# Performance work log

Measured on AMD Instinct MI355X. Metric: run time of the kernel, lower is better.

The kernel has to match this reference:

```python
import jax, jax.numpy as jnp
import numpy as np

B, XDIM, TWIN, INCH = 1024, 62, 10, 128
MID, OUT, K, K1, LIN, HC = 256, 512, 3, 10, 512, 4
EPS = 1e-5

REGIONS = [
    list(range(0, 5)),
    list(range(5, 8)) + list(range(14, 17)),
    list(range(8, 11)) + list(range(17, 20)),
    list(range(11, 14)) + list(range(20, 23)),
    list(range(23, 26)) + list(range(32, 35)),
    list(range(26, 29)) + list(range(35, 38)),
    list(range(29, 32)) + list(range(38, 41)),
    list(range(41, 44)) + list(range(50, 52)) + list(range(57, 58)),
    list(range(44, 47)) + list(range(52, 55)) + list(range(58, 61)),
    list(range(47, 50)) + list(range(55, 57)) + list(range(61, 62)),
]


def setup_inputs() -> dict:
    key = jax.random.key(0)
    ks = jax.random.split(key, 40)
    n = lambda k, s, sc=0.02: jax.random.normal(k, s, jnp.float32) * sc
    inp = {
        "x": jax.random.normal(ks[0], (B, XDIM, TWIN, INCH), jnp.float32),
        "tfe_w": n(ks[1], (XDIM, TWIN)),          # depthwise Conv2d (10,1) weight, squeezed
        "tfe_b": jnp.zeros((XDIM,), jnp.float32),
        "cheby1_w": n(ks[2], (K, INCH, OUT)),
        "A": n(ks[3], (XDIM, XDIM)),
        "cheby2_w": n(ks[4], (K, MID, OUT)),
        "A1": n(ks[5], (K1, K1)),
        "b_gate": jnp.float32(1.0),
        "c_gate": jnp.float32(1.0),
        "region_b": jnp.zeros((K1, MID), jnp.float32),
        "hc_w1": n(ks[6], (OUT * 72, LIN)),
        "hc_b1": jnp.zeros((LIN,), jnp.float32),
        "bn1_g": jnp.ones((LIN,), jnp.float32),
        "bn1_b": jnp.zeros((LIN,), jnp.float32),
        "hc_w2": n(ks[7], (LIN, LIN // 2)),
        "hc_b2": jnp.zeros((LIN // 2,), jnp.float32),
        "bn2_g": jnp.ones((LIN // 2,), jnp.float32),
        "bn2_b": jnp.zeros((LIN // 2,), jnp.float32),
        "hc_w3": n(ks[8], (LIN // 2, HC)),
        "hc_b3": jnp.zeros((HC,), jnp.float32),
    }
    for i, idx in enumerate(REGIONS):
        inp[f"rw{i+1}"] = n(ks[10 + i], (MID, INCH, len(idx)))
    return inp


def _cheby(x, L, Ws):
    # sum_k  S_k @ x @ W_k  with S_0 = I, S_k = S_{k-1} @ L ; then ReLU
    S = jnp.eye(L.shape[0], dtype=x.dtype)
    res = jnp.zeros(x.shape[:2] + (Ws.shape[-1],), x.dtype)
    for k in range(Ws.shape[0]):
        res = res + jnp.einsum("nm,bmt,to->bno", S, x, Ws[k])
        S = S @ L
    return jax.nn.relu(res)


def _bn(h, g, b):
    mu = h.mean(axis=0)
    v = h.var(axis=0)  # biased, training-mode BatchNorm1d
    return (h - mu) * jax.lax.rsqrt(v + EPS) * g + b


def _forward(x, tfe_w, tfe_b, cheby1_w, A, cheby2_w, A1, b_gate, c_gate,
             rw1, rw2, rw3, rw4, rw5, rw6, rw7, rw8, rw9, rw10, region_b,
             hc_w1, hc_b1, bn1_g, bn1_b, hc_w2, hc_b2, bn2_g, bn2_b, hc_w3, hc_b3):
    # variance gate (torch.var default: unbiased)
    sigma = jnp.var(x, axis=2, ddof=1)                              # (B, 62, INCH)
    g_tfe = jnp.einsum("bcit,ci->bct", x, tfe_w) + tfe_b[None, :, None]
    g = g_tfe * jnp.exp(-sigma)                                      # (B, 62, INCH)

    g1 = _cheby(g, A, cheby1_w)                                      # (B, 62, OUT)

    rws = [rw1, rw2, rw3, rw4, rw5, rw6, rw7, rw8, rw9, rw10]
    RG = []
    for i, (idx, w) in enumerate(zip(REGIONS, rws)):
        reg = g[:, jnp.asarray(idx), :]                              # (B, L, INCH)
        RG.append(jnp.einsum("blc,mcl->bm", reg, w) + region_b[i])   # Conv1d, full-width kernel
    g2in = jnp.stack(RG, axis=1)                                     # (B, 10, MID)
    g2 = _cheby(g2in, A1, cheby2_w)                                  # (B, 10, OUT)

    att = jnp.concatenate([b_gate * g1, c_gate * g2], axis=1)        # (B, 72, OUT)
    cat = jnp.concatenate([g1, g2], axis=1)
    out = jax.nn.softmax(att, axis=1) * cat
    out = out.reshape(out.shape[0], -1)                              # (B, 72*OUT)

    h = jax.nn.gelu(_bn(out @ hc_w1 + hc_b1, bn1_g, bn1_b), approximate=False)
    h = jax.nn.gelu(_bn(h @ hc_w2 + hc_b2, bn2_g, bn2_b), approximate=False)
    h = h @ hc_w3 + hc_b3
    return jax.nn.softmax(h, axis=1)


def reference(x, tfe_w, tfe_b, cheby1_w, A, cheby2_w, A1, b_gate, c_gate,
              rw1, rw2, rw3, rw4, rw5, rw6, rw7, rw8, rw9, rw10, region_b,
              hc_w1, hc_b1, bn1_g, bn1_b, hc_w2, hc_b2, bn2_g, bn2_b, hc_w3, hc_b3):
    return _forward(x, tfe_w, tfe_b, cheby1_w, A, cheby2_w, A1, b_gate, c_gate,
                    rw1, rw2, rw3, rw4, rw5, rw6, rw7, rw8, rw9, rw10, region_b,
                    hc_w1, hc_b1, bn1_g, bn1_b, hc_w2, hc_b2, bn2_g, bn2_b, hc_w3, hc_b3)
```

## Files before the change

### kernel.cpp

```cpp
#include <hip/hip_runtime.h>
#include <math.h>


__constant__ int cOrder[62] = {
  0,1,2,3,4,
  5,6,7,14,15,16,
  8,9,10,17,18,19,
  11,12,13,20,21,22,
  23,24,25,32,33,34,
  26,27,28,35,36,37,
  29,30,31,38,39,40,
  41,42,43,50,51,57,
  44,45,46,52,53,54,58,59,60,
  47,48,49,55,56,61
};
__constant__ int cPos[62] = {
  0,1,2,3,4, 5,6,7, 11,12,13, 17,18,19, 8,9,10, 14,15,16, 20,21,22,
  23,24,25, 29,30,31, 35,36,37, 26,27,28, 32,33,34, 38,39,40,
  41,42,43, 47,48,49, 56,57,58, 44,45, 50,51,52, 59,60, 46, 53,54,55, 61
};
__constant__ int cRegK[10]   = {640,768,768,768,768,768,768,768,1152,768};
__constant__ int cRegCum[10] = {0,640,1408,2176,2944,3712,4480,5248,6016,7168};

struct Ptr10 { const float* p[10]; };

typedef __attribute__((ext_vector_type(8))) short bf16x8;
typedef __attribute__((ext_vector_type(4))) float f32x4;

__device__ __forceinline__ float gelu_exact(float v){
  return 0.5f * v * (1.0f + erff(v * 0.70710678118654752f));
}
__device__ __forceinline__ unsigned short f2bf(float f){
  unsigned u = __float_as_uint(f);
  unsigned r = (u + 0x7fffu + ((u >> 16) & 1u)) >> 16;
  return (unsigned short)r;
}
__device__ __forceinline__ float bf2f(unsigned short u){
  return __uint_as_float(((unsigned)u) << 16);
}
__device__ __forceinline__ void load_lds16(const unsigned short* g, unsigned short* l){
  __builtin_amdgcn_global_load_lds(
      (const __attribute__((address_space(1))) void*)g,
      (__attribute__((address_space(3))) void*)l, 16, 0, 0);
}

template<bool RELU>
__global__ __launch_bounds__(256) void k_mfma(
    const unsigned short* __restrict__ A, long lda,
    const unsigned short* __restrict__ BT, long ldb,
    void* __restrict__ Cv, int ldc, int kPerZ, long cStrideZ, int mcCount){
  __shared__ unsigned short As[128*32];
  __shared__ unsigned short Bs[128*32];
  int mt, nt, zt;
  if (mcCount){
    int id = blockIdx.x;
    int c = ((id >> 6) << 3) + (id & 7);
    int member = (id >> 3) & 7;
    zt = c / mcCount;
    int mc = c - zt*mcCount;
    mt = mc*2 + (member >> 2);
    nt = member & 3;
  } else { mt = blockIdx.x; nt = blockIdx.y; zt = blockIdx.z; }
  int tid = threadIdx.x;
  int wave = tid >> 6, lane = tid & 63;
  int m0 = mt * 128, n0 = nt * 128;
  int kStart = zt * kPerZ;
  int waveM = wave >> 1, waveN = wave & 1;
  int lr = lane >> 2, ch = lane & 3;
  int quad = lane >> 4, mrow = lane & 15;
  int swe = ((quad ^ (mrow & 3)) << 3);

  int rA0 = wave*32 + lr;
  int rA1 = rA0 + 16;
  int ce  = ((ch ^ (rA0 & 3)) << 3);
  const unsigned short* gA0 = A  + (long)(m0 + rA0)*lda + kStart + ce;
  const unsigned short* gA1 = A  + (long)(m0 + rA1)*lda + kStart + ce;
  const unsigned short* gB0 = BT + (long)(n0 + rA0)*ldb + kStart + ce;
  const unsigned short* gB1 = BT + (long)(n0 + rA1)*ldb + kStart + ce;
  unsigned short* lA0 = &As[(wave*32)*32];
  unsigned short* lA1 = &As[(wave*32+16)*32];
  unsigned short* lB0 = &Bs[(wave*32)*32];
  unsigned short* lB1 = &Bs[(wave*32+16)*32];

  f32x4 acc[4][4] = {};
  int nIter = kPerZ >> 5;
  for (int it = 0; it < nIter; ++it){
    long ko = (long)it << 5;
    load_lds16(gA0 + ko, lA0);
    load_lds16(gA1 + ko, lA1);
    load_lds16(gB0 + ko, lB0);
    load_lds16(gB1 + ko, lB1);
    __syncthreads();
    bf16x8 af[4], bfr[4];
#pragma unroll
    for (int mi = 0; mi < 4; mi++)
      af[mi] = *(const bf16x8*)&As[(waveM*64 + mi*16 + mrow)*32 + swe];
#pragma unroll
    for (int ni = 0; ni < 4; ni++)
      bfr[ni] = *(const bf16x8*)&Bs[(waveN*64 + ni*16 + mrow)*32 + swe];
#pragma unroll
    for (int mi = 0; mi < 4; mi++)
#pragma unroll
      for (int ni = 0; ni < 4; ni++)
        acc[mi][ni] = __builtin_amdgcn_mfma_f32_16x16x32_bf16(
            af[mi], bfr[ni], acc[mi][ni], 0, 0, 0);
    __syncthreads();
  }
  if (RELU){
    unsigned short* C = (unsigned short*)Cv;
#pragma unroll
    for (int mi = 0; mi < 4; mi++)
#pragma unroll
      for (int ni = 0; ni < 4; ni++){
        int col = n0 + waveN*64 + ni*16 + mrow;
#pragma unroll
        for (int r = 0; r < 4; r++){
          int row = m0 + waveM*64 + mi*16 + quad*4 + r;
          C[(long)row*ldc + col] = f2bf(fmaxf(acc[mi][ni][r], 0.f));
        }
      }
  } else {
    float* C = (float*)Cv + (long)zt * cStrideZ;
#pragma unroll
    for (int mi = 0; mi < 4; mi++)
#pragma unroll
      for (int ni = 0; ni < 4; ni++){
        int col = n0 + waveN*64 + ni*16 + mrow;
#pragma unroll
        for (int r = 0; r < 4; r++){
          int row = m0 + waveM*64 + mi*16 + quad*4 + r;
          C[(long)row*ldc + col] = acc[mi][ni][r];
        }
      }
  }
}
template __global__ void k_mfma<true>(const unsigned short*, long, const unsigned short*, long, void*, int, int, long, int);
template __global__ void k_mfma<false>(const unsigned short*, long, const unsigned short*, long, void*, int, int, long, int);

__global__ __launch_bounds__(256) void k_mfma_region(
    const unsigned short* __restrict__ ARb,
    const unsigned short* __restrict__ RWT,
    const float* __restrict__ regb, float* __restrict__ g2in){
  __shared__ unsigned short As[128*32];
  __shared__ unsigned short Bs[128*32];
  int z = blockIdx.z;
  int K = cRegK[z];
  int cumk = cRegCum[z];
  const unsigned short* A  = ARb + cumk;
  const unsigned short* BT = RWT + (long)cumk*256;
  long lda = 7936, ldb = K;
  int tid = threadIdx.x;
  int wave = tid >> 6, lane = tid & 63;
  int m0 = blockIdx.x * 128, n0 = blockIdx.y * 128;
  int waveM = wave >> 1, waveN = wave & 1;
  int lr = lane >> 2, ch = lane & 3;
  int quad = lane >> 4, mrow = lane & 15;
  int swe = ((quad ^ (mrow & 3)) << 3);

  int rA0 = wave*32 + lr;
  int rA1 = rA0 + 16;
  int ce  = ((ch ^ (rA0 & 3)) << 3);
  const unsigned short* gA0 = A  + (long)(m0 + rA0)*lda + ce;
  const unsigned short* gA1 = A  + (long)(m0 + rA1)*lda + ce;
  const unsigned short* gB0 = BT + (long)(n0 + rA0)*ldb + ce;
  const unsigned short* gB1 = BT + (long)(n0 + rA1)*ldb + ce;
  unsigned short* lA0 = &As[(wave*32)*32];
  unsigned short* lA1 = &As[(wave*32+16)*32];
  unsigned short* lB0 = &Bs[(wave*32)*32];
  unsigned short* lB1 = &Bs[(wave*32+16)*32];

  f32x4 acc[4][4] = {};
  int nIter = K >> 5;
  for (int it = 0; it < nIter; ++it){
    long ko = (long)it << 5;
    load_lds16(gA0 + ko, lA0);
    load_lds16(gA1 + ko, lA1);
    load_lds16(gB0 + ko, lB0);
    load_lds16(gB1 + ko, lB1);
    __syncthreads();
    bf16x8 af[4], bfr[4];
#pragma unroll
    for (int mi = 0; mi < 4; mi++)
      af[mi] = *(const bf16x8*)&As[(waveM*64 + mi*16 + mrow)*32 + swe];
#pragma unroll
    for (int ni = 0; ni < 4; ni++)
      bfr[ni] = *(const bf16x8*)&Bs[(waveN*64 + ni*16 + mrow)*32 + swe];
#pragma unroll
    for (int mi = 0; mi < 4; mi++)
#pragma unroll
      for (int ni = 0; ni < 4; ni++)
        acc[mi][ni] = __builtin_amdgcn_mfma_f32_16x16x32_bf16(
            af[mi], bfr[ni], acc[mi][ni], 0, 0, 0);
    __syncthreads();
  }
#pragma unroll
  for (int mi = 0; mi < 4; mi++)
#pragma unroll
    for (int ni = 0; ni < 4; ni++){
      int col = n0 + waveN*64 + ni*16 + mrow;
      float bias = regb[z*256 + col];
#pragma unroll
      for (int r = 0; r < 4; r++){
        int row = m0 + waveM*64 + mi*16 + quad*4 + r;
        g2in[(long)row*2560 + z*256 + col] = acc[mi][ni][r] + bias;
      }
    }
}

__global__ __launch_bounds__(256) void k_front(
    const float* __restrict__ s0, unsigned short* __restrict__ d0,
    const float* __restrict__ s1, unsigned short* __restrict__ d1,
    const float* __restrict__ s2, unsigned short* __restrict__ d2,
    const float* __restrict__ s3, unsigned short* __restrict__ d3,
    Ptr10 rws, unsigned short* __restrict__ RWT,
    const float* __restrict__ Amat, float* __restrict__ AT,
    float* __restrict__ A2T,
    const float* __restrict__ x, const float* __restrict__ tw,
    const float* __restrict__ tb, unsigned short* __restrict__ arb,
    unsigned short* __restrict__ xcat, float* __restrict__ sumz){
  __shared__ float smem[64*65];
  int id = blockIdx.x;
  int tid = threadIdx.x;
  if (id >= 15342){
    *(float4*)(sumz + tid*4) = make_float4(0.f,0.f,0.f,0.f);
    return;
  }
  if (id >= 7406){
    int q = id - 7406;
    int r = tid >> 5, j = tid & 31;
    int idx = q*8 + r;
    int b = idx / 62, n = idx - b*62;
    const float4* xp = (const float4*)(x + (long)idx*1280) + j;
    float sx=0.f,sy=0.f,sz=0.f,sw=0.f;
    float qx=0.f,qy=0.f,qz=0.f,qw=0.f;
    float gx=0.f,gy=0.f,gz=0.f,gw=0.f;
#pragma unroll
    for (int i = 0; i < 10; i++){
      float4 v = xp[i*32];
      float w = tw[n*10+i];
      sx+=v.x; sy+=v.y; sz+=v.z; sw+=v.w;
      qx=fmaf(v.x,v.x,qx); qy=fmaf(v.y,v.y,qy);
      qz=fmaf(v.z,v.z,qz); qw=fmaf(v.w,v.w,qw);
      gx=fmaf(v.x,w,gx); gy=fmaf(v.y,w,gy);
      gz=fmaf(v.z,w,gz); gw=fmaf(v.w,w,gw);
    }
    float tbn = tb[n];
    float mx_=sx*0.1f, my_=sy*0.1f, mz_=sz*0.1f, mw_=sw*0.1f;
    float rx = (gx+tbn)*expf(-(qx-10.f*mx_*mx_)*(1.f/9.f));
    float ry = (gy+tbn)*expf(-(qy-10.f*my_*my_)*(1.f/9.f));
    float rz = (gz+tbn)*expf(-(qz-10.f*mz_*mz_)*(1.f/9.f));
    float rw = (gw+tbn)*expf(-(qw-10.f*mw_*mw_)*(1.f/9.f));
    ushort4 u = make_ushort4(f2bf(rx), f2bf(ry), f2bf(rz), f2bf(rw));
    *(ushort4*)(arb  + (long)b*7936  + cPos[n]*128 + j*4) = u;
    *(ushort4*)(xcat + (long)b*23808 + n*384       + j*4) = u;
    return;
  }
  if (id < 7344 && id >= 4784){
    int q = id - 4784;
    int z = q >> 8, m = q & 255;
    int K = cRegK[z], L = K >> 7;
    const float* rw = rws.p[z] + (long)m*K;
    unsigned short* dst = RWT + (long)cRegCum[z]*256 + (long)m*K;
    for (int i = tid; i < K; i += 256) smem[i] = rw[i];
    __syncthreads();
    for (int k = tid; k < K; k += 256){
      int l = k >> 7, c = k & 127;
      dst[k] = f2bf(smem[c*L + l]);
    }
    return;
  }
  if (id >= 7344){
    int r = id - 7344, c = tid;
    if (c < 62) smem[c] = Amat[r*62 + c];
    __syncthreads();
    if (c < 62){
      AT[c*62 + r] = smem[c];
      float s = 0.f;
      for (int t = 0; t < 62; t++) s = fmaf(smem[t], Amat[t*62 + c], s);
      A2T[c*62 + r] = s;
    }
    return;
  }
  const float* src; unsigned short* dst; int R, C, rt, ct;
  if (id < 4608){ src=s0; dst=d0; R=36864; C=512; rt=id>>3;  ct=id&7; }
  else if (id < 4640){ int q=id-4608; src=s1; dst=d1; R=512; C=256; rt=q>>2; ct=q&3; }
  else if (id < 4688){ int q=id-4640; src=s2; dst=d2; R=384; C=512; rt=q>>3; ct=q&7; }
  else { int q=id-4688; src=s3; dst=d3; R=768; C=512; rt=q>>3; ct=q&7; }
  int r0 = rt*64, c0 = ct*64;
  int rr = tid >> 2, cb = (tid & 3) << 2;
#pragma unroll
  for (int i = 0; i < 4; i++){
    int cc = cb + i*16;
    float4 v = *(const float4*)(src + (long)(r0+rr)*C + c0 + cc);
    smem[rr*65+cc+0]=v.x; smem[rr*65+cc+1]=v.y;
    smem[rr*65+cc+2]=v.z; smem[rr*65+cc+3]=v.w;
  }
  __syncthreads();
  int cc = tid >> 2, rb = (tid & 3) << 2;
#pragma unroll
  for (int i = 0; i < 4; i++){
    int r = rb + i*16;
    ushort4 u = make_ushort4(f2bf(smem[(r+0)*65+cc]), f2bf(smem[(r+1)*65+cc]),
                             f2bf(smem[(r+2)*65+cc]), f2bf(smem[(r+3)*65+cc]));
    *(ushort4*)(dst + (long)(c0+cc)*R + r0 + r) = u;
  }
}

__global__ __launch_bounds__(256) void k_spread2(
    const unsigned short* __restrict__ ARb, const float* __restrict__ AT,
    const float* __restrict__ A2T, unsigned short* __restrict__ xcat){
  __shared__ float sgn[7936];
  int b = blockIdx.x, tid = threadIdx.x;
  for (int i = tid; i < 7936; i += 256){
    int p = i >> 7, c = i & 127;
    sgn[cOrder[p]*128 + c] = bf2f(ARb[(long)b*7936 + i]);
  }
  __syncthreads();
  int c = tid & 127, mat = tid >> 7;
  const float* MT = mat ? A2T : AT;
  float acc[62];
#pragma unroll
  for (int n = 0; n < 62; n++) acc[n] = 0.f;
  for (int m = 0; m < 62; m++){
    float gv = sgn[m*128 + c];
    const float* Mp = MT + m*62;
#pragma unroll
    for (int n = 0; n < 62; n++) acc[n] = fmaf(Mp[n], gv, acc[n]);
  }
  long base = (long)b*23808 + (mat+1)*128 + c;
#pragma unroll
  for (int n = 0; n < 62; n++) xcat[base + (long)n*384] = f2bf(acc[n]);
}

__global__ __launch_bounds__(256) void k_x2cat(
    const float* __restrict__ g2in, const float* __restrict__ A1,
    unsigned short* __restrict__ X2){
  __shared__ float sg[2560];
  __shared__ float sA1[100];
  __shared__ float sA2[100];
  int b = blockIdx.x, tid = threadIdx.x;
  for (int i = tid; i < 2560; i += 256) sg[i] = g2in[(long)b*2560 + i];
  if (tid < 100) sA1[tid] = A1[tid];
  __syncthreads();
  if (tid < 100){
    int n = tid/10, m = tid - n*10;
    float a = 0.f;
#pragma unroll
    for (int t = 0; t < 10; t++) a = fmaf(sA1[n*10+t], sA1[t*10+m], a);
    sA2[tid] = a;
  }
  __syncthreads();
  for (int i = tid; i < 2560; i += 256){
    int n = i >> 8, t = i & 255;
    float v1 = 0.f, v2 = 0.f;
#pragma unroll
    for (int m = 0; m < 10; m++){
      float gv = sg[(m<<8) + t];
      v1 = fmaf(sA1[n*10+m], gv, v1);
      v2 = fmaf(sA2[n*10+m], gv, v2);
    }
    long base = (long)b*7680 + n*768;
    X2[base + t]       = f2bf(sg[i]);
    X2[base + 256 + t] = f2bf(v1);
    X2[base + 512 + t] = f2bf(v2);
  }
}

__global__ __launch_bounds__(256) void k_softcat(
    const unsigned short* __restrict__ g1, const unsigned short* __restrict__ g2,
    const float* __restrict__ bg_, const float* __restrict__ cg_,
    unsigned short* __restrict__ outb){
  int b = blockIdx.x;
  int o = blockIdx.y*256 + threadIdx.x;
  float v[72];
  const unsigned short* p1 = g1 + (long)b*62*512 + o;
#pragma unroll
  for (int j = 0; j < 62; j++) v[j] = bf2f(p1[j*512]);
  const unsigned short* p2 = g2 + (long)b*10*512 + o;
#pragma unroll
  for (int j = 0; j < 10; j++) v[62+j] = bf2f(p2[j*512]);
  float bg = *bg_, cg = *cg_;
  float mx = -1e30f;
#pragma unroll
  for (int j = 0; j < 72; j++){
    float av = (j < 62 ? bg : cg) * v[j];
    mx = fmaxf(mx, av);
  }
  float sum = 0.f;
#pragma unroll
  for (int j = 0; j < 72; j++){
    float e = expf((j < 62 ? bg : cg) * v[j] - mx);
    sum += e;
    v[j] = e * v[j];
  }
  float inv = 1.f / sum;
  unsigned short* op = outb + (long)b*36864 + o;
#pragma unroll
  for (int j = 0; j < 72; j++) op[j*512] = f2bf(v[j] * inv);
}

__global__ __launch_bounds__(256) void k_reduce_stats(
    const float4* __restrict__ P, float4* __restrict__ h1,
    float* __restrict__ sum, float* __restrict__ ssq){
  __shared__ float4 ls[128], ls2[128];
  int c  = threadIdx.x & 127;
  int rr = threadIdx.x >> 7;
  int r0 = blockIdx.x * 8;
  float4 s1 = make_float4(0.f,0.f,0.f,0.f);
  float4 s2 = make_float4(0.f,0.f,0.f,0.f);
#pragma unroll
  for (int k = 0; k < 4; k++){
    int row = r0 + rr + 2*k;
    long idx = (long)row*128 + c;
    float4 v = make_float4(0.f,0.f,0.f,0.f);
#pragma unroll
    for (int s = 0; s < 16; s++){
      float4 p = P[(long)s*131072 + idx];
      v.x += p.x; v.y += p.y; v.z += p.z; v.w += p.w;
    }
    h1[idx] = v;
    s1.x += v.x; s1.y += v.y; s1.z += v.z; s1.w += v.w;
    s2.x = fmaf(v.x,v.x,s2.x); s2.y = fmaf(v.y,v.y,s2.y);
    s2.z = fmaf(v.z,v.z,s2.z); s2.w = fmaf(v.w,v.w,s2.w);
  }
  if (rr){ ls[c] = s1; ls2[c] = s2; }
  __syncthreads();
  if (!rr){
    float4 o1 = ls[c], o2 = ls2[c];
    atomicAdd(&sum[c*4+0], s1.x+o1.x); atomicAdd(&sum[c*4+1], s1.y+o1.y);
    atomicAdd(&sum[c*4+2], s1.z+o1.z); atomicAdd(&sum[c*4+3], s1.w+o1.w);
    atomicAdd(&ssq[c*4+0], s2.x+o2.x); atomicAdd(&ssq[c*4+1], s2.y+o2.y);
    atomicAdd(&ssq[c*4+2], s2.z+o2.z); atomicAdd(&ssq[c*4+3], s2.w+o2.w);
  }
}

__global__ __launch_bounds__(256) void k_bngelu(
    const float* __restrict__ h1, const float* __restrict__ sum,
    const float* __restrict__ ssq, const float* __restrict__ gam,
    const float* __restrict__ bet, unsigned short* __restrict__ h1b){
  int base = (blockIdx.x*256 + threadIdx.x) * 4;
  int j = base & 511;
  float4 v = *(const float4*)(h1 + base);
  float mu0 = sum[j+0]*(1.f/1024.f), mu1 = sum[j+1]*(1.f/1024.f);
  float mu2 = sum[j+2]*(1.f/1024.f), mu3 = sum[j+3]*(1.f/1024.f);
  float rs0 = rsqrtf(ssq[j+0]*(1.f/1024.f) - mu0*mu0 + 1e-5f);
  float rs1 = rsqrtf(ssq[j+1]*(1.f/1024.f) - mu1*mu1 + 1e-5f);
  float rs2 = rsqrtf(ssq[j+2]*(1.f/1024.f) - mu2*mu2 + 1e-5f);
  float rs3 = rsqrtf(ssq[j+3]*(1.f/1024.f) - mu3*mu3 + 1e-5f);
  ushort4 u;
  u.x = f2bf(gelu_exact((v.x - mu0)*rs0*gam[j+0] + bet[j+0]));
  u.y = f2bf(gelu_exact((v.y - mu1)*rs1*gam[j+1] + bet[j+1]));
  u.z = f2bf(gelu_exact((v.z - mu2)*rs2*gam[j+2] + bet[j+2]));
  u.w = f2bf(gelu_exact((v.w - mu3)*rs3*gam[j+3] + bet[j+3]));
  *(ushort4*)(h1b + base) = u;
}

__global__ __launch_bounds__(256) void k_stats2r(
    const float* __restrict__ P2, float* __restrict__ h2,
    float* __restrict__ mu, float* __restrict__ rs){
  __shared__ float lsm[256], lss[256];
  int j0 = blockIdx.x * 8;
  int jj = threadIdx.x & 7, bg = threadIdx.x >> 3;
  float s = 0.f, s2 = 0.f;
#pragma unroll 4
  for (int it = 0; it < 32; it++){
    int row = it*32 + bg;
    float v = 0.f;
#pragma unroll
    for (int sp = 0; sp < 4; sp++)
      v += P2[((long)sp*1024 + row)*256 + j0 + jj];
    h2[(long)row*256 + j0 + jj] = v;
    s += v; s2 = fmaf(v, v, s2);
  }
  lsm[threadIdx.x] = s; lss[threadIdx.x] = s2;
  __syncthreads();
  if (threadIdx.x < 8){
    float a = lsm[threadIdx.x], a2 = lss[threadIdx.x];
    for (int g = 1; g < 32; g++){ a += lsm[g*8 + threadIdx.x]; a2 += lss[g*8 + threadIdx.x]; }
    float m = a * (1.f/1024.f);
    float var = a2 * (1.f/1024.f) - m*m;
    mu[j0 + threadIdx.x] = m;
    rs[j0 + threadIdx.x] = rsqrtf(var + 1e-5f);
  }
}

__global__ __launch_bounds__(256) void k_final(
    const float* __restrict__ h2, const float* __restrict__ mu,
    const float* __restrict__ rs, const float* __restrict__ gam,
    const float* __restrict__ bet, const float* __restrict__ w3,
    const float* __restrict__ b3, float* __restrict__ outp){
  int b = blockIdx.x, tid = threadIdx.x;
  float v = h2[(long)b*256 + tid];
  v = (v - mu[tid]) * rs[tid] * gam[tid] + bet[tid];
  v = gelu_exact(v);
  float4 w = ((const float4*)w3)[tid];
  float p0 = v*w.x, p1 = v*w.y, p2 = v*w.z, p3 = v*w.w;
#pragma unroll
  for (int o = 32; o > 0; o >>= 1){
    p0 += __shfl_down(p0, o);
    p1 += __shfl_down(p1, o);
    p2 += __shfl_down(p2, o);
    p3 += __shfl_down(p3, o);
  }
  __shared__ float red[4][4];
  int wv = tid >> 6;
  if ((tid & 63) == 0){ red[wv][0]=p0; red[wv][1]=p1; red[wv][2]=p2; red[wv][3]=p3; }
  __syncthreads();
  if (tid == 0){
    float l[4];
#pragma unroll
    for (int c = 0; c < 4; c++)
      l[c] = red[0][c]+red[1][c]+red[2][c]+red[3][c] + b3[c];
    float m = fmaxf(fmaxf(l[0], l[1]), fmaxf(l[2], l[3]));
    float e[4]; float sum = 0.f;
#pragma unroll
    for (int c = 0; c < 4; c++){ e[c] = expf(l[c]-m); sum += e[c]; }
    float inv = 1.f / sum;
#pragma unroll
    for (int c = 0; c < 4; c++) outp[(long)b*4 + c] = e[c]*inv;
  }
}

extern "C" void kernel_launch(void* const* d_in, const int* in_sizes, int n_in,
                              void* d_out, int out_size, void* d_ws, size_t ws_size,
                              hipStream_t stream){
  (void)n_in; (void)out_size; (void)ws_size;
  bool dictOrder = (in_sizes[9] == 2560);
  const float* x     = (const float*)d_in[0];
  const float* tfe_w = (const float*)d_in[1];
  const float* tfe_b = (const float*)d_in[2];
  const float* ch1w  = (const float*)d_in[3];
  const float* Amat  = (const float*)d_in[4];
  const float* ch2w  = (const float*)d_in[5];
  const float* A1mat = (const float*)d_in[6];
  const float* bgate = (const float*)d_in[7];
  const float* cgate = (const float*)d_in[8];
  const float* regb  = (const float*)d_in[dictOrder ? 9 : 19];
  int o = dictOrder ? 0 : 10;
  const float* hc_w1 = (const float*)d_in[10+o];
  const float* bn1g  = (const float*)d_in[12+o];
  const float* bn1b  = (const float*)d_in[13+o];
  const float* hc_w2 = (const float*)d_in[14+o];
  const float* bn2g  = (const float*)d_in[16+o];
  const float* bn2b  = (const float*)d_in[17+o];
  const float* hc_w3 = (const float*)d_in[18+o];
  const float* hc_b3 = (const float*)d_in[19+o];
  Ptr10 rws;
  for (int i = 0; i < 10; i++) rws.p[i] = (const float*)d_in[(dictOrder ? 20 : 9) + i];

  char* Wb = (char*)d_ws;
  unsigned short* ARb   = (unsigned short*)(Wb + 0);
  unsigned short* XCAT  = (unsigned short*)(Wb + 16252928);
  unsigned short* RWT   = (unsigned short*)(Wb + 65011712);
  float*          G2IN  = (float*)(Wb + 69074944);
  unsigned short* X2CAT = (unsigned short*)(Wb + 79560704);
  unsigned short* W1T   = (unsigned short*)(Wb + 95289344);
  unsigned short* WC1T  = (unsigned short*)(Wb + 133038080);
  unsigned short* WC2T  = (unsigned short*)(Wb + 133431296);
  unsigned short* G1    = (unsigned short*)(Wb + 134217728);
  unsigned short* G2    = (unsigned short*)(Wb + 199229440);
  unsigned short* OUTB  = (unsigned short*)(Wb + 0);
  float*          P     = (float*)(Wb + 209715200);
  float*          H1    = (float*)(Wb + 243269632);
  float*          H2    = (float*)(Wb + 245366784);
  float*          SUM1  = (float*)(Wb + 246415360);
  float*          SSQ1  = SUM1 + 512;
  float*          MU2   = SUM1 + 1024;
  float*          RS2   = SUM1 + 1280;
  float*          AT    = (float*)(Wb + 246423552);
  float*          A2T   = (float*)(Wb + 246439040);
  unsigned short* W2T   = (unsigned short*)(Wb + 246454528);
  unsigned short* H1B   = (unsigned short*)(Wb + 246716928);

  k_front<<<15343, 256, 0, stream>>>(hc_w1, W1T, hc_w2, W2T, ch1w, WC1T,
                                     ch2w, WC2T, rws, RWT, Amat, AT, A2T,
                                     x, tfe_w, tfe_b, ARb, XCAT, SUM1);
  k_spread2<<<1024, 256, 0, stream>>>(ARb, AT, A2T, XCAT);
  k_mfma_region<<<dim3(8,2,10), 256, 0, stream>>>(ARb, RWT, regb, G2IN);
  k_x2cat<<<1024, 256, 0, stream>>>(G2IN, A1mat, X2CAT);
  k_mfma<true><<<320, 256, 0, stream>>>(X2CAT, 768, WC2T, 768, (void*)G2, 512, 768, 0, 40);
  k_mfma<true><<<1984, 256, 0, stream>>>(XCAT, 384, WC1T, 384, (void*)G1, 512, 384, 0, 248);
  k_softcat<<<dim3(1024,2), 256, 0, stream>>>(G1, G2, bgate, cgate, OUTB);
  k_mfma<false><<<512, 256, 0, stream>>>(OUTB, 36864, W1T, 36864, (void*)P, 512, 2304, 524288, 4);
  k_reduce_stats<<<128, 256, 0, stream>>>((const float4*)P, (float4*)H1, SUM1, SSQ1);
  k_bngelu<<<512, 256, 0, stream>>>(H1, SUM1, SSQ1, bn1g, bn1b, H1B);
  k_mfma<false><<<dim3(8,2,4), 256, 0, stream>>>(H1B, 512, W2T, 512, (void*)P, 256, 128, 262144, 0);
  k_stats2r<<<32, 256, 0, stream>>>(P, H2, MU2, RS2);
  k_final<<<1024, 256, 0, stream>>>(H2, MU2, RS2, bn2g, bn2b, hc_w3, hc_b3, (float*)d_out);
}
```

Baseline: 917.1 us.

## Merge independent launches and fuse BatchNorm tails with grid-wide atomic barriers

Merges spread2 and the region GEMM into one launch, and merges the two Chebyshev GEMMs into one dual launch with grouped tile ordering. It also fuses stats reduction with BN+GELU, and BN2 with the final linear and softmax, using atomic counters as grid-wide barriers. The aim is to cut kernel launches, drop the H1/H2 intermediate round-trips and fill the GPU better. The spin-wait barriers depend on every block being resident at once, which risks deadlock if they are not, and k_front now also zeroes the counters.

```diff
diff --git a/kernel.cpp b/kernel.cpp
--- a/kernel.cpp
+++ b/kernel.cpp
@@ -137,21 +137,128 @@
 template __global__ void k_mfma<true>(const unsigned short*, long, const unsigned short*, long, void*, int, int, long, int);
 template __global__ void k_mfma<false>(const unsigned short*, long, const unsigned short*, long, void*, int, int, long, int);
 
-__global__ __launch_bounds__(256) void k_mfma_region(
-    const unsigned short* __restrict__ ARb,
-    const unsigned short* __restrict__ RWT,
-    const float* __restrict__ regb, float* __restrict__ g2in){
+__global__ __launch_bounds__(256) void k_dual(
+    const unsigned short* __restrict__ A2c, const unsigned short* __restrict__ B2c,
+    unsigned short* __restrict__ C2c,
+    const unsigned short* __restrict__ A1c, const unsigned short* __restrict__ B1c,
+    unsigned short* __restrict__ C1c){
   __shared__ unsigned short As[128*32];
   __shared__ unsigned short Bs[128*32];
-  int z = blockIdx.z;
+  int id = blockIdx.x;
+  bool is1 = id >= 320;
+  const unsigned short* A  = is1 ? A1c : A2c;
+  const unsigned short* BT = is1 ? B1c : B2c;
+  unsigned short* C = is1 ? C1c : C2c;
+  long lda = is1 ? 384 : 768;
+  long ldb = lda;
+  int kPerZ = (int)lda;
+  if (is1) id -= 320;
+  int c = ((id >> 6) << 3) + (id & 7);
+  int member = (id >> 3) & 7;
+  int mt = c*2 + (member >> 2);
+  int nt = member & 3;
+  int tid = threadIdx.x;
+  int wave = tid >> 6, lane = tid & 63;
+  int m0 = mt * 128, n0 = nt * 128;
+  int waveM = wave >> 1, waveN = wave & 1;
+  int lr = lane >> 2, ch = lane & 3;
+  int quad = lane >> 4, mrow = lane & 15;
+  int swe = ((quad ^ (mrow & 3)) << 3);
+
+  int rA0 = wave*32 + lr;
+  int rA1 = rA0 + 16;
+  int ce  = ((ch ^ (rA0 & 3)) << 3);
+  const unsigned short* gA0 = A  + (long)(m0 + rA0)*lda + ce;
+  const unsigned short* gA1 = A  + (long)(m0 + rA1)*lda + ce;
+  const unsigned short* gB0 = BT + (long)(n0 + rA0)*ldb + ce;
+  const unsigned short* gB1 = BT + (long)(n0 + rA1)*ldb + ce;
+  unsigned short* lA0 = &As[(wave*32)*32];
+  unsigned short* lA1 = &As[(wave*32+16)*32];
+  unsigned short* lB0 = &Bs[(wave*32)*32];
+  unsigned short* lB1 = &Bs[(wave*32+16)*32];
+
+  f32x4 acc[4][4] = {};
+  int nIter = kPerZ >> 5;
+  for (int it = 0; it < nIter; ++it){
+    long ko = (long)it << 5;
+    load_lds16(gA0 + ko, lA0);
+    load_lds16(gA1 + ko, lA1);
+    load_lds16(gB0 + ko, lB0);
+    load_lds16(gB1 + ko, lB1);
+    __syncthreads();
+    bf16x8 af[4], bfr[4];
+#pragma unroll
+    for (int mi = 0; mi < 4; mi++)
+      af[mi] = *(const bf16x8*)&As[(waveM*64 + mi*16 + mrow)*32 + swe];
+#pragma unroll
+    for (int ni = 0; ni < 4; ni++)
+      bfr[ni] = *(const bf16x8*)&Bs[(waveN*64 + ni*16 + mrow)*32 + swe];
+#pragma unroll
+    for (int mi = 0; mi < 4; mi++)
+#pragma unroll
+      for (int ni = 0; ni < 4; ni++)
+        acc[mi][ni] = __builtin_amdgcn_mfma_f32_16x16x32_bf16(
+            af[mi], bfr[ni], acc[mi][ni], 0, 0, 0);
+    __syncthreads();
+  }
+#pragma unroll
+  for (int mi = 0; mi < 4; mi++)
+#pragma unroll
+    for (int ni = 0; ni < 4; ni++){
+      int col = n0 + waveN*64 + ni*16 + mrow;
+#pragma unroll
+      for (int r = 0; r < 4; r++){
+        int row = m0 + waveM*64 + mi*16 + quad*4 + r;
+        C[(long)row*512 + col] = f2bf(fmaxf(acc[mi][ni][r], 0.f));
+      }
+    }
+}
+
+__global__ __launch_bounds__(256) void k_mid(
+    const unsigned short* __restrict__ ARb, const float* __restrict__ AT,
+    const float* __restrict__ A2T, unsigned short* __restrict__ xcat,
+    const unsigned short* __restrict__ RWT, const float* __restrict__ regb,
+    float* __restrict__ g2in){
+  __shared__ __align__(16) char smraw[32768];
+  int id = blockIdx.x;
+  int tid = threadIdx.x;
+  if (id < 1024){
+    float* sgn = (float*)smraw;
+    int b = id;
+    for (int i = tid; i < 7936; i += 256){
+      int p = i >> 7, c = i & 127;
+      sgn[cOrder[p]*128 + c] = bf2f(ARb[(long)b*7936 + i]);
+    }
+    __syncthreads();
+    int c = tid & 127, mat = tid >> 7;
+    const float* MT = mat ? A2T : AT;
+    float acc[62];
+#pragma unroll
+    for (int n = 0; n < 62; n++) acc[n] = 0.f;
+    for (int m = 0; m < 62; m++){
+      float gv = sgn[m*128 + c];
+      const float* Mp = MT + m*62;
+#pragma unroll
+      for (int n = 0; n < 62; n++) acc[n] = fmaf(Mp[n], gv, acc[n]);
+    }
+    long base = (long)b*23808 + (mat+1)*128 + c;
+#pragma unroll
+    for (int n = 0; n < 62; n++) xcat[base + (long)n*384] = f2bf(acc[n]);
+    return;
+  }
+  unsigned short* As = (unsigned short*)smraw;
+  unsigned short* Bs = As + 128*32;
+  int id2 = id - 1024;
+  int z = id2 >> 4;
+  int m  = id2 & 15;
+  int mt = m >> 1, nt = m & 1;
   int K = cRegK[z];
   int cumk = cRegCum[z];
   const unsigned short* A  = ARb + cumk;
   const unsigned short* BT = RWT + (long)cumk*256;
   long lda = 7936, ldb = K;
-  int tid = threadIdx.x;
   int wave = tid >> 6, lane = tid & 63;
-  int m0 = blockIdx.x * 128, n0 = blockIdx.y * 128;
+  int m0 = mt * 128, n0 = nt * 128;
   int waveM = wave >> 1, waveN = wave & 1;
   int lr = lane >> 2, ch = lane & 3;
   int quad = lane >> 4, mrow = lane & 15;
@@ -222,7 +329,7 @@
   int id = blockIdx.x;
   int tid = threadIdx.x;
   if (id >= 15342){
-    *(float4*)(sumz + tid*4) = make_float4(0.f,0.f,0.f,0.f);
+    *(float4*)(sumz + (id-15342)*1024 + tid*4) = make_float4(0.f,0.f,0.f,0.f);
     return;
   }
   if (id >= 7406){
@@ -306,32 +413,6 @@
   }
 }
 
-__global__ __launch_bounds__(256) void k_spread2(
-    const unsigned short* __restrict__ ARb, const float* __restrict__ AT,
-    const float* __restrict__ A2T, unsigned short* __restrict__ xcat){
-  __shared__ float sgn[7936];
-  int b = blockIdx.x, tid = threadIdx.x;
-  for (int i = tid; i < 7936; i += 256){
-    int p = i >> 7, c = i & 127;
-    sgn[cOrder[p]*128 + c] = bf2f(ARb[(long)b*7936 + i]);
-  }
-  __syncthreads();
-  int c = tid & 127, mat = tid >> 7;
-  const float* MT = mat ? A2T : AT;
-  float acc[62];
-#pragma unroll
-  for (int n = 0; n < 62; n++) acc[n] = 0.f;
-  for (int m = 0; m < 62; m++){
-    float gv = sgn[m*128 + c];
-    const float* Mp = MT + m*62;
-#pragma unroll
-    for (int n = 0; n < 62; n++) acc[n] = fmaf(Mp[n], gv, acc[n]);
-  }
-  long base = (long)b*23808 + (mat+1)*128 + c;
-#pragma unroll
-  for (int n = 0; n < 62; n++) xcat[base + (long)n*384] = f2bf(acc[n]);
-}
-
 __global__ __launch_bounds__(256) void k_x2cat(
     const float* __restrict__ g2in, const float* __restrict__ A1,
     unsigned short* __restrict__ X2){
@@ -399,13 +480,17 @@
   for (int j = 0; j < 72; j++) op[j*512] = f2bf(v[j] * inv);
 }
 
-__global__ __launch_bounds__(256) void k_reduce_stats(
-    const float4* __restrict__ P, float4* __restrict__ h1,
-    float* __restrict__ sum, float* __restrict__ ssq){
+__global__ __launch_bounds__(256) void k_tail1(
+    const float4* __restrict__ P, const float* __restrict__ gam,
+    const float* __restrict__ bet, float* __restrict__ sum,
+    float* __restrict__ ssq, unsigned int* __restrict__ cnt,
+    unsigned short* __restrict__ h1b){
   __shared__ float4 ls[128], ls2[128];
-  int c  = threadIdx.x & 127;
-  int rr = threadIdx.x >> 7;
+  int tid = threadIdx.x;
+  int c  = tid & 127;
+  int rr = tid >> 7;
   int r0 = blockIdx.x * 8;
+  float4 va[4];
   float4 s1 = make_float4(0.f,0.f,0.f,0.f);
   float4 s2 = make_float4(0.f,0.f,0.f,0.f);
 #pragma unroll
@@ -418,7 +503,7 @@
       float4 p = P[(long)s*131072 + idx];
       v.x += p.x; v.y += p.y; v.z += p.z; v.w += p.w;
     }
-    h1[idx] = v;
+    va[k] = v;
     s1.x += v.x; s1.y += v.y; s1.z += v.z; s1.w += v.w;
     s2.x = fmaf(v.x,v.x,s2.x); s2.y = fmaf(v.y,v.y,s2.y);
     s2.z = fmaf(v.z,v.z,s2.z); s2.w = fmaf(v.w,v.w,s2.w);
@@ -432,92 +517,110 @@
     atomicAdd(&ssq[c*4+0], s2.x+o2.x); atomicAdd(&ssq[c*4+1], s2.y+o2.y);
     atomicAdd(&ssq[c*4+2], s2.z+o2.z); atomicAdd(&ssq[c*4+3], s2.w+o2.w);
   }
-}
-
-__global__ __launch_bounds__(256) void k_bngelu(
-    const float* __restrict__ h1, const float* __restrict__ sum,
-    const float* __restrict__ ssq, const float* __restrict__ gam,
-    const float* __restrict__ bet, unsigned short* __restrict__ h1b){
-  int base = (blockIdx.x*256 + threadIdx.x) * 4;
-  int j = base & 511;
-  float4 v = *(const float4*)(h1 + base);
-  float mu0 = sum[j+0]*(1.f/1024.f), mu1 = sum[j+1]*(1.f/1024.f);
-  float mu2 = sum[j+2]*(1.f/1024.f), mu3 = sum[j+3]*(1.f/1024.f);
-  float rs0 = rsqrtf(ssq[j+0]*(1.f/1024.f) - mu0*mu0 + 1e-5f);
-  float rs1 = rsqrtf(ssq[j+1]*(1.f/1024.f) - mu1*mu1 + 1e-5f);
-  float rs2 = rsqrtf(ssq[j+2]*(1.f/1024.f) - mu2*mu2 + 1e-5f);
-  float rs3 = rsqrtf(ssq[j+3]*(1.f/1024.f) - mu3*mu3 + 1e-5f);
-  ushort4 u;
-  u.x = f2bf(gelu_exact((v.x - mu0)*rs0*gam[j+0] + bet[j+0]));
-  u.y = f2bf(gelu_exact((v.y - mu1)*rs1*gam[j+1] + bet[j+1]));
-  u.z = f2bf(gelu_exact((v.z - mu2)*rs2*gam[j+2] + bet[j+2]));
-  u.w = f2bf(gelu_exact((v.w - mu3)*rs3*gam[j+3] + bet[j+3]));
-  *(ushort4*)(h1b + base) = u;
-}
-
-__global__ __launch_bounds__(256) void k_stats2r(
-    const float* __restrict__ P2, float* __restrict__ h2,
-    float* __restrict__ mu, float* __restrict__ rs){
-  __shared__ float lsm[256], lss[256];
-  int j0 = blockIdx.x * 8;
-  int jj = threadIdx.x & 7, bg = threadIdx.x >> 3;
+  __threadfence();
+  __syncthreads();
+  if (tid == 0){
+    __hip_atomic_fetch_add(cnt, 1u, __ATOMIC_RELEASE, __HIP_MEMORY_SCOPE_AGENT);
+    while (__hip_atomic_load(cnt, __ATOMIC_ACQUIRE, __HIP_MEMORY_SCOPE_AGENT) < 128u)
+      __builtin_amdgcn_s_sleep(16);
+  }
+  __syncthreads();
+  int j = c*4;
+  float mu0 = __hip_atomic_load(&sum[j+0], __ATOMIC_RELAXED, __HIP_MEMORY_SCOPE_AGENT)*(1.f/1024.f);
+  float mu1 = __hip_atomic_load(&sum[j+1], __ATOMIC_RELAXED, __HIP_MEMORY_SCOPE_AGENT)*(1.f/1024.f);
+  float mu2 = __hip_atomic_load(&sum[j+2], __ATOMIC_RELAXED, __HIP_MEMORY_SCOPE_AGENT)*(1.f/1024.f);
+  float mu3 = __hip_atomic_load(&sum[j+3], __ATOMIC_RELAXED, __HIP_MEMORY_SCOPE_AGENT)*(1.f/1024.f);
+  float q0 = __hip_atomic_load(&ssq[j+0], __ATOMIC_RELAXED, __HIP_MEMORY_SCOPE_AGENT);
+  float q1 = __hip_atomic_load(&ssq[j+1], __ATOMIC_RELAXED, __HIP_MEMORY_SCOPE_AGENT);
+  float q2 = __hip_atomic_load(&ssq[j+2], __ATOMIC_RELAXED, __HIP_MEMORY_SCOPE_AGENT);
+  float q3 = __hip_atomic_load(&ssq[j+3], __ATOMIC_RELAXED, __HIP_MEMORY_SCOPE_AGENT);
+  float rs0 = rsqrtf(q0*(1.f/1024.f) - mu0*mu0 + 1e-5f);
+  float rs1 = rsqrtf(q1*(1.f/1024.f) - mu1*mu1 + 1e-5f);
+  float rs2 = rsqrtf(q2*(1.f/1024.f) - mu2*mu2 + 1e-5f);
+  float rs3 = rsqrtf(q3*(1.f/1024.f) - mu3*mu3 + 1e-5f);
+  float g0 = gam[j+0], g1 = gam[j+1], g2 = gam[j+2], g3 = gam[j+3];
+  float b0 = bet[j+0], b1 = bet[j+1], b2 = bet[j+2], b3 = bet[j+3];
+#pragma unroll
+  for (int k = 0; k < 4; k++){
+    int row = r0 + rr + 2*k;
+    float4 v = va[k];
+    ushort4 u;
+    u.x = f2bf(gelu_exact((v.x - mu0)*rs0*g0 + b0));
+    u.y = f2bf(gelu_exact((v.y - mu1)*rs1*g1 + b1));
+    u.z = f2bf(gelu_exact((v.z - mu2)*rs2*g2 + b2));
+    u.w = f2bf(gelu_exact((v.w - mu3)*rs3*g3 + b3));
+    *(ushort4*)(h1b + (long)row*512 + j) = u;
+  }
+}
+
+__global__ __launch_bounds__(256) void k_tail2(
+    const float* __restrict__ P2, const float* __restrict__ gam,
+    const float* __restrict__ bet, const float* __restrict__ w3,
+    const float* __restrict__ b3, float* __restrict__ sum,
+    float* __restrict__ ssq, unsigned int* __restrict__ cnt,
+    float* __restrict__ outp){
+  __shared__ float lv[32][257];
+  __shared__ float rd[32][8][4];
+  int tid = threadIdx.x;
+  int rbase = blockIdx.x * 32;
+  float v[32];
   float s = 0.f, s2 = 0.f;
-#pragma unroll 4
-  for (int it = 0; it < 32; it++){
-    int row = it*32 + bg;
-    float v = 0.f;
+#pragma unroll 8
+  for (int r = 0; r < 32; r++){
+    int row = rbase + r;
+    float a = 0.f;
 #pragma unroll
     for (int sp = 0; sp < 4; sp++)
-      v += P2[((long)sp*1024 + row)*256 + j0 + jj];
-    h2[(long)row*256 + j0 + jj] = v;
-    s += v; s2 = fmaf(v, v, s2);
-  }
-  lsm[threadIdx.x] = s; lss[threadIdx.x] = s2;
-  __syncthreads();
-  if (threadIdx.x < 8){
-    float a = lsm[threadIdx.x], a2 = lss[threadIdx.x];
-    for (int g = 1; g < 32; g++){ a += lsm[g*8 + threadIdx.x]; a2 += lss[g*8 + threadIdx.x]; }
-    float m = a * (1.f/1024.f);
-    float var = a2 * (1.f/1024.f) - m*m;
-    mu[j0 + threadIdx.x] = m;
-    rs[j0 + threadIdx.x] = rsqrtf(var + 1e-5f);
-  }
-}
-
-__global__ __launch_bounds__(256) void k_final(
-    const float* __restrict__ h2, const float* __restrict__ mu,
-    const float* __restrict__ rs, const float* __restrict__ gam,
-    const float* __restrict__ bet, const float* __restrict__ w3,
-    const float* __restrict__ b3, float* __restrict__ outp){
-  int b = blockIdx.x, tid = threadIdx.x;
-  float v = h2[(long)b*256 + tid];
-  v = (v - mu[tid]) * rs[tid] * gam[tid] + bet[tid];
-  v = gelu_exact(v);
-  float4 w = ((const float4*)w3)[tid];
-  float p0 = v*w.x, p1 = v*w.y, p2 = v*w.z, p3 = v*w.w;
-#pragma unroll
-  for (int o = 32; o > 0; o >>= 1){
-    p0 += __shfl_down(p0, o);
-    p1 += __shfl_down(p1, o);
-    p2 += __shfl_down(p2, o);
-    p3 += __shfl_down(p3, o);
-  }
-  __shared__ float red[4][4];
-  int wv = tid >> 6;
-  if ((tid & 63) == 0){ red[wv][0]=p0; red[wv][1]=p1; red[wv][2]=p2; red[wv][3]=p3; }
+      a += P2[((long)sp*1024 + row)*256 + tid];
+    v[r] = a;
+    s += a; s2 = fmaf(a, a, s2);
+  }
+  atomicAdd(&sum[tid], s);
+  atomicAdd(&ssq[tid], s2);
+  __threadfence();
   __syncthreads();
   if (tid == 0){
+    __hip_atomic_fetch_add(cnt, 1u, __ATOMIC_RELEASE, __HIP_MEMORY_SCOPE_AGENT);
+    while (__hip_atomic_load(cnt, __ATOMIC_ACQUIRE, __HIP_MEMORY_SCOPE_AGENT) < 32u)
+      __builtin_amdgcn_s_sleep(16);
+  }
+  __syncthreads();
+  float mu = __hip_atomic_load(&sum[tid], __ATOMIC_RELAXED, __HIP_MEMORY_SCOPE_AGENT)*(1.f/1024.f);
+  float qq = __hip_atomic_load(&ssq[tid], __ATOMIC_RELAXED, __HIP_MEMORY_SCOPE_AGENT);
+  float rs = rsqrtf(qq*(1.f/1024.f) - mu*mu + 1e-5f);
+  float gm = gam[tid], bt = bet[tid];
+#pragma unroll 8
+  for (int r = 0; r < 32; r++)
+    lv[r][tid] = gelu_exact((v[r] - mu)*rs*gm + bt);
+  __syncthreads();
+  int row = tid >> 3, seg = tid & 7;
+  float p0=0.f,p1=0.f,p2=0.f,p3=0.f;
+#pragma unroll
+  for (int i = 0; i < 32; i++){
+    int cc = seg*32 + i;
+    float a = lv[row][cc];
+    float4 w = ((const float4*)w3)[cc];
+    p0 = fmaf(a, w.x, p0); p1 = fmaf(a, w.y, p1);
+    p2 = fmaf(a, w.z, p2); p3 = fmaf(a, w.w, p3);
+  }
+  rd[row][seg][0]=p0; rd[row][seg][1]=p1; rd[row][seg][2]=p2; rd[row][seg][3]=p3;
+  __syncthreads();
+  if (tid < 32){
     float l[4];
 #pragma unroll
-    for (int c = 0; c < 4; c++)
-      l[c] = red[0][c]+red[1][c]+red[2][c]+red[3][c] + b3[c];
+    for (int c = 0; c < 4; c++){
+      float a = 0.f;
+#pragma unroll
+      for (int g = 0; g < 8; g++) a += rd[tid][g][c];
+      l[c] = a + b3[c];
+    }
     float m = fmaxf(fmaxf(l[0], l[1]), fmaxf(l[2], l[3]));
-    float e[4]; float sum = 0.f;
-#pragma unroll
-    for (int c = 0; c < 4; c++){ e[c] = expf(l[c]-m); sum += e[c]; }
-    float inv = 1.f / sum;
-#pragma unroll
-    for (int c = 0; c < 4; c++) outp[(long)b*4 + c] = e[c]*inv;
+    float e[4]; float su = 0.f;
+#pragma unroll
+    for (int c = 0; c < 4; c++){ e[c] = expf(l[c]-m); su += e[c]; }
+    float inv = 1.f / su;
+#pragma unroll
+    for (int c = 0; c < 4; c++) outp[(long)(rbase+tid)*4 + c] = e[c]*inv;
   }
 }
 
@@ -561,30 +664,26 @@
   unsigned short* G2    = (unsigned short*)(Wb + 199229440);
   unsigned short* OUTB  = (unsigned short*)(Wb + 0);
   float*          P     = (float*)(Wb + 209715200);
-  float*          H1    = (float*)(Wb + 243269632);
-  float*          H2    = (float*)(Wb + 245366784);
   float*          SUM1  = (float*)(Wb + 246415360);
   float*          SSQ1  = SUM1 + 512;
-  float*          MU2   = SUM1 + 1024;
-  float*          RS2   = SUM1 + 1280;
+  float*          SUM2  = SUM1 + 1024;
+  float*          SSQ2  = SUM1 + 1280;
+  unsigned int*   CNT1  = (unsigned int*)(SUM1 + 1536);
+  unsigned int*   CNT2  = (unsigned int*)(SUM1 + 1537);
   float*          AT    = (float*)(Wb + 246423552);
   float*          A2T   = (float*)(Wb + 246439040);
   unsigned short* W2T   = (unsigned short*)(Wb + 246454528);
   unsigned short* H1B   = (unsigned short*)(Wb + 246716928);
 
-  k_front<<<15343, 256, 0, stream>>>(hc_w1, W1T, hc_w2, W2T, ch1w, WC1T,
+  k_front<<<15344, 256, 0, stream>>>(hc_w1, W1T, hc_w2, W2T, ch1w, WC1T,
                                      ch2w, WC2T, rws, RWT, Amat, AT, A2T,
                                      x, tfe_w, tfe_b, ARb, XCAT, SUM1);
-  k_spread2<<<1024, 256, 0, stream>>>(ARb, AT, A2T, XCAT);
-  k_mfma_region<<<dim3(8,2,10), 256, 0, stream>>>(ARb, RWT, regb, G2IN);
+  k_mid<<<1184, 256, 0, stream>>>(ARb, AT, A2T, XCAT, RWT, regb, G2IN);
   k_x2cat<<<1024, 256, 0, stream>>>(G2IN, A1mat, X2CAT);
-  k_mfma<true><<<320, 256, 0, stream>>>(X2CAT, 768, WC2T, 768, (void*)G2, 512, 768, 0, 40);
-  k_mfma<true><<<1984, 256, 0, stream>>>(XCAT, 384, WC1T, 384, (void*)G1, 512, 384, 0, 248);
+  k_dual<<<2304, 256, 0, stream>>>(X2CAT, WC2T, G2, XCAT, WC1T, G1);
   k_softcat<<<dim3(1024,2), 256, 0, stream>>>(G1, G2, bgate, cgate, OUTB);
   k_mfma<false><<<512, 256, 0, stream>>>(OUTB, 36864, W1T, 36864, (void*)P, 512, 2304, 524288, 4);
-  k_reduce_stats<<<128, 256, 0, stream>>>((const float4*)P, (float4*)H1, SUM1, SSQ1);
-  k_bngelu<<<512, 256, 0, stream>>>(H1, SUM1, SSQ1, bn1g, bn1b, H1B);
+  k_tail1<<<128, 256, 0, stream>>>((const float4*)P, bn1g, bn1b, SUM1, SSQ1, CNT1, H1B);
   k_mfma<false><<<dim3(8,2,4), 256, 0, stream>>>(H1B, 512, W2T, 512, (void*)P, 256, 128, 262144, 0);
-  k_stats2r<<<32, 256, 0, stream>>>(P, H2, MU2, RS2);
-  k_final<<<1024, 256, 0, stream>>>(H2, MU2, RS2, bn2g, bn2b, hc_w3, hc_b3, (float*)d_out);
-}
+  k_tail2<<<32, 256, 0, stream>>>(P, bn2g, bn2b, hc_w3, hc_b3, SUM2, SSQ2, CNT2, (float*)d_out);
+}
```

New measurement: 883.1 us. 3.7% less time.
